# Optimization experiments

Hardware: AMD Instinct MI355X
Metric: run time of the kernel (lower is better)

## Reference

```python
import jax, jax.numpy as jnp
import numpy as np

B, S = 2, 2048
Q_DIM, KV_DIM = 2048, 2048
N_HEADS, HEAD_DIM = 16, 128
N_KV_HEADS = 4            # kv_bandwidth 512 // head_dim 128
N_REP = N_HEADS // N_KV_HEADS
EPS = 1e-5


def setup_inputs() -> dict:
    key = jax.random.key(0)
    ks = jax.random.split(key, 6)
    return {
        "q_stream": jax.random.normal(ks[0], (B, S, Q_DIM), jnp.float32),
        "kv_stream": jax.random.normal(ks[1], (B, S, KV_DIM), jnp.float32),
        "wq": jax.random.normal(ks[2], (Q_DIM, N_HEADS * HEAD_DIM), jnp.float32) * 0.02,
        "wk": jax.random.normal(ks[3], (KV_DIM, N_KV_HEADS * HEAD_DIM), jnp.float32) * 0.02,
        "wv": jax.random.normal(ks[4], (KV_DIM, N_KV_HEADS * HEAD_DIM), jnp.float32) * 0.02,
        "wo": jax.random.normal(ks[5], (N_HEADS * HEAD_DIM, Q_DIM), jnp.float32) * 0.02,
        "q_norm_w": jnp.ones((HEAD_DIM,), jnp.float32),
        "k_norm_w": jnp.ones((HEAD_DIM,), jnp.float32),
    }


def _rmsnorm(x, w):
    # RMSNorm over the last (head_dim) axis
    var = jnp.mean(x * x, axis=-1, keepdims=True)
    return x * jax.lax.rsqrt(var + EPS) * w


def reference(q_stream, kv_stream, wq, wk, wv, wo, q_norm_w, k_norm_w):
    b, s, _ = q_stream.shape
    # QKV projections (weights stored [in, out])
    xq = jnp.einsum("bsd,de->bse", q_stream, wq).reshape(b, s, N_HEADS, HEAD_DIM)
    xk = jnp.einsum("bsd,de->bse", kv_stream, wk).reshape(b, s, N_KV_HEADS, HEAD_DIM)
    xv = jnp.einsum("bsd,de->bse", kv_stream, wv).reshape(b, s, N_KV_HEADS, HEAD_DIM)
    # qk_norm_mode == "before_rope": per-head RMSNorm on q and k
    xq = _rmsnorm(xq, q_norm_w)
    xk = _rmsnorm(xk, k_norm_w)
    # GQA: repeat kv heads to match query heads
    k = jnp.repeat(xk, N_REP, axis=2)  # [b, s, H, D]
    v = jnp.repeat(xv, N_REP, axis=2)
    # causal scaled-dot-product attention
    scale = 1.0 / np.sqrt(HEAD_DIM).astype(np.float32)
    scores = jnp.einsum("bqhd,bkhd->bhqk", xq, k) * scale  # [b, H, S, S]
    causal = jnp.tril(jnp.ones((s, s), dtype=bool))
    scores = jnp.where(causal, scores, jnp.finfo(scores.dtype).min)
    probs = jax.nn.softmax(scores, axis=-1)
    out = jnp.einsum("bhqk,bkhd->bqhd", probs, v).reshape(b, s, N_HEADS * HEAD_DIM)
    return jnp.einsum("bse,eo->bso", out, wo)
```

## Files before the change

### kernel.cpp

```cpp
#include <hip/hip_runtime.h>
#include <cstdint>


using bf16 = __bf16;
using bf16x4 = __attribute__((ext_vector_type(4))) __bf16;
using bf16x8 = __attribute__((ext_vector_type(8))) __bf16;
using s16x4  = __attribute__((ext_vector_type(4))) short;
using f32x4  = __attribute__((ext_vector_type(4))) float;

#define SEQ 2048
#define NH 16
#define NKVH 4
#define HD 128

#define NEG (-3.0e38f)

#if defined(__has_builtin)
#if __has_builtin(__builtin_amdgcn_mfma_f32_16x16x16bf16_1k)
#define HAVE_1K 1
#endif
#endif
__device__ __forceinline__ f32x4 mfma_16x16x16(bf16x4 a, bf16x4 b, f32x4 c) {
#ifdef HAVE_1K
    return __builtin_amdgcn_mfma_f32_16x16x16bf16_1k(
        __builtin_bit_cast(s16x4, a), __builtin_bit_cast(s16x4, b), c, 0, 0, 0);
#else
    f32x4 d;
    asm volatile("v_mfma_f32_16x16x16_bf16 %0, %1, %2, %3"
                 : "=v"(d) : "v"(a), "v"(b), "v"(c));
    return d;
#endif
}

__device__ __forceinline__ float fast_exp2(float x) {
#if defined(__has_builtin)
#if __has_builtin(__builtin_amdgcn_exp2f)
    return __builtin_amdgcn_exp2f(x);
#else
    return exp2f(x);
#endif
#else
    return exp2f(x);
#endif
}

__device__ __forceinline__ void load_lds16(const bf16* g, bf16* l) {
    __builtin_amdgcn_global_load_lds(
        (const __attribute__((address_space(1))) unsigned int*)g,
        (__attribute__((address_space(3))) unsigned int*)l, 16, 0, 0);
}

__global__ __launch_bounds__(256) void cvt_f32_bf16(const float* __restrict__ in,
                                                    bf16* __restrict__ out, int n8) {
    int i = blockIdx.x * 256 + threadIdx.x;
    if (i >= n8) return;
    const float4* p = (const float4*)in + (long)i * 2;
    float4 f0 = p[0], f1 = p[1];
    bf16x8 o = {(bf16)f0.x, (bf16)f0.y, (bf16)f0.z, (bf16)f0.w,
                (bf16)f1.x, (bf16)f1.y, (bf16)f1.z, (bf16)f1.w};
    *((bf16x8*)out + i) = o;
}

__global__ void transpose2d(const float* __restrict__ in, bf16* __restrict__ out,
                            int R, int C) {
    __shared__ bf16 tile[32][33];
    int x  = blockIdx.x * 32 + threadIdx.x;
    int y0 = blockIdx.y * 32 + threadIdx.y;
#pragma unroll
    for (int i = 0; i < 32; i += 8) {
        int y = y0 + i;
        if (y < R && x < C) tile[threadIdx.y + i][threadIdx.x] = (bf16)in[(long)y * C + x];
    }
    __syncthreads();
    int ox  = blockIdx.y * 32 + threadIdx.x;
    int oy0 = blockIdx.x * 32 + threadIdx.y;
#pragma unroll
    for (int i = 0; i < 32; i += 8) {
        int oy = oy0 + i;
        if (oy < C && ox < R) out[(long)oy * R + ox] = tile[threadIdx.x][threadIdx.y + i];
    }
}

template <typename CT>
__global__ __launch_bounds__(256) void gemm_bt(const bf16* __restrict__ A,
                                               const bf16* __restrict__ BT,
                                               CT* __restrict__ C,
                                               int M, int N, int K) {
    __shared__ bf16 As[2][128][32];
    __shared__ bf16 Bs[2][128][32];
    const int tid  = threadIdx.x;
    const int wave = tid >> 6, lane = tid & 63;
    const int nwg = gridDim.x * gridDim.y;
    const int bid = blockIdx.y * gridDim.x + blockIdx.x;
    const int swz = (bid & 7) * (nwg >> 3) + (bid >> 3);
    const int bx = swz % gridDim.x, by = swz / gridDim.x;
    const int m0 = by * 128, n0 = bx * 128;
    const int wm = (wave >> 1) * 64, wn = (wave & 1) * 64;
    const int lrow = lane & 15, quad = lane >> 4;
    const int lko = quad * 8;

    const bf16* ga0 = A  + (long)(m0 + (tid >> 2)) * K + (tid & 3) * 8;
    const bf16* ga1 = ga0 + 64L * K;
    const bf16* gb0 = BT + (long)(n0 + (tid >> 2)) * K + (tid & 3) * 8;
    const bf16* gb1 = gb0 + 64L * K;
    bf16* la0 = &As[0][0][0] + tid * 8;
    bf16* lb0 = &Bs[0][0][0] + tid * 8;

    f32x4 acc[4][4] = {};

    const int nIt = K >> 5;
    load_lds16(ga0, la0);
    load_lds16(ga1, la0 + 2048);
    load_lds16(gb0, lb0);
    load_lds16(gb1, lb0 + 2048);
    __syncthreads();

#pragma unroll 1
    for (int it = 0; it < nIt; ++it) {
        const int cur = it & 1;
        if (it + 1 < nIt) {
            const int k0 = (it + 1) * 32;
            bf16* la = la0 + (cur ^ 1) * 4096;
            bf16* lb = lb0 + (cur ^ 1) * 4096;
            load_lds16(ga0 + k0, la);
            load_lds16(ga1 + k0, la + 2048);
            load_lds16(gb0 + k0, lb);
            load_lds16(gb1 + k0, lb + 2048);
        }
        bf16x8 af[4], bfr[4];
#pragma unroll
        for (int i = 0; i < 4; ++i) af[i]  = *(const bf16x8*)(&As[cur][wm + i * 16 + lrow][lko]);
#pragma unroll
        for (int j = 0; j < 4; ++j) bfr[j] = *(const bf16x8*)(&Bs[cur][wn + j * 16 + lrow][lko]);
#pragma unroll
        for (int i = 0; i < 4; ++i)
#pragma unroll
            for (int j = 0; j < 4; ++j)
                acc[i][j] = __builtin_amdgcn_mfma_f32_16x16x32_bf16(af[i], bfr[j], acc[i][j], 0, 0, 0);
        __syncthreads();
    }
#pragma unroll
    for (int i = 0; i < 4; ++i) {
        int mrow0 = m0 + wm + i * 16 + quad * 4;
#pragma unroll
        for (int j = 0; j < 4; ++j) {
            int ncol = n0 + wn + j * 16 + lrow;
#pragma unroll
            for (int r = 0; r < 4; ++r)
                C[(long)(mrow0 + r) * N + ncol] = (CT)acc[i][j][r];
        }
    }
}

__global__ __launch_bounds__(256) void rmsnorm_head(bf16* __restrict__ X,
                                                    const float* __restrict__ W,
                                                    int nvec, int lhpr, int stride) {
    int v = blockIdx.x * 4 + (threadIdx.x >> 6);
    int lane = threadIdx.x & 63;
    if (v >= nvec) return;
    int row = v >> lhpr, head = v & ((1 << lhpr) - 1);
    bf16* x = X + (long)row * stride + head * HD;
    float fa = (float)x[lane * 2], fb = (float)x[lane * 2 + 1];
    float ss = fa * fa + fb * fb;
#pragma unroll
    for (int off = 1; off < 64; off <<= 1) ss += __shfl_xor(ss, off, 64);
    float r = rsqrtf(ss * (1.0f / 128.0f) + 1e-5f);
    x[lane * 2]     = (bf16)(fa * r * W[lane * 2]);
    x[lane * 2 + 1] = (bf16)(fb * r * W[lane * 2 + 1]);
}

__global__ __launch_bounds__(256) void repack_k(const bf16* __restrict__ xkv,
                                                bf16* __restrict__ kf) {
    int kt = blockIdx.x, kvh = blockIdx.y, b = blockIdx.z;
    int tid = threadIdx.x, lane = tid & 63, ks = tid >> 6;
    int lrow = lane & 15, quad = lane >> 4;
    const bf16* src = xkv + ((long)b * SEQ + kt * 64) * 1024 + kvh * HD;
    bf16* dst = kf + ((long)((b * NKVH + kvh) * 32 + kt)) * 8192;
#pragma unroll
    for (int nt = 0; nt < 4; ++nt) {
        bf16x8 v = *(const bf16x8*)(src + (long)(nt * 16 + lrow) * 1024 + ks * 32 + quad * 8);
        *(bf16x8*)(dst + ((nt * 4 + ks) * 64 + lane) * 8) = v;
    }
}

__global__ __launch_bounds__(256) void repack_v(const bf16* __restrict__ xkv,
                                                bf16* __restrict__ vf) {
    __shared__ bf16 Vls[64][136];
    int kt = blockIdx.x, kvh = blockIdx.y, b = blockIdx.z;
    int tid = threadIdx.x;
    const bf16* src = xkv + ((long)b * SEQ + kt * 64) * 1024 + 512 + kvh * HD;
#pragma unroll
    for (int p = 0; p < 4; ++p) {
        int c = p * 256 + tid;
        int r = c >> 4, dc = (c & 15) * 8;
        *(uint4*)(&Vls[r][dc]) = *(const uint4*)(src + (long)r * 1024 + dc);
    }
    __syncthreads();
    int lane = tid & 63, w = tid >> 6, lrow = lane & 15, quad = lane >> 4;
    bf16* dst = vf + ((long)((b * NKVH + kvh) * 32 + kt)) * 8192;
#pragma unroll
    for (int nt = 0; nt < 4; ++nt)
#pragma unroll
        for (int dtl = 0; dtl < 2; ++dtl) {
            int dt = w * 2 + dtl;
            bf16x4 v = {Vls[nt * 16 + quad * 4 + 0][dt * 16 + lrow],
                        Vls[nt * 16 + quad * 4 + 1][dt * 16 + lrow],
                        Vls[nt * 16 + quad * 4 + 2][dt * 16 + lrow],
                        Vls[nt * 16 + quad * 4 + 3][dt * 16 + lrow]};
            *(bf16x4*)(dst + ((nt * 8 + dt) * 64 + lane) * 4) = v;
        }
}

__global__ __launch_bounds__(512, 4) void attn_kernel(const bf16* __restrict__ Q,
                                                      const bf16* __restrict__ KF,
                                                      const bf16* __restrict__ VF,
                                                      bf16* __restrict__ O) {
    __shared__ bf16 Kf[2][8192];
    __shared__ bf16 Vf[2][8192];
    const int tid = threadIdx.x, wave = tid >> 6, lane = tid & 63;
    const int w4 = wave & 3, grpW = wave >> 2;
    const int bid = blockIdx.x;
    const int grp = bid & 7;
    const int b = grp >> 2, kvh = grp & 3;
    const int slot = bid >> 3;
    const int pr = slot & 15;
    const int h = kvh * 4 + (slot >> 4);
    const int lrow = lane & 15, quad = lane >> 4;
    const float scl2 = 0.12751744f;
    const float THR = 62.7f;

    const int qt1 = 31 - pr, qt2 = pr;

    const bf16* kfb = KF + ((long)(b * NKVH + kvh) * 32) * 8192;
    const bf16* vfb = VF + ((long)(b * NKVH + kvh) * 32) * 8192;

    auto stage = [&](int pair, int bsel) {
        const bf16* kg = kfb + (long)pair * 8192 + tid * 8;
        const bf16* vg = vfb + (long)pair * 8192 + tid * 8;
        bf16* kd = &Kf[bsel][0] + tid * 8;
        bf16* vd = &Vf[bsel][0] + tid * 8;
        load_lds16(kg, kd);
        load_lds16(kg + 4096, kd + 4096);
        load_lds16(vg, vd);
        load_lds16(vg + 4096, vd + 4096);
    };

    float m_i = NEG, l_i = 0.f;
    f32x4 oT[8] = {};
    bf16x8 bqw[4];

    auto combine_write_reset = [&](int qrow) {
        float a1keep = 0.f;
        float* vs = (float*)&Vf[0][0];
        const int sl = w4 * 64 + lane;
        __syncthreads();
        if (grpW == 1) {
            float* d = vs + sl * 18;
#pragma unroll
            for (int dt = 0; dt < 4; ++dt)
#pragma unroll
                for (int r = 0; r < 4; ++r) d[dt * 4 + r] = oT[dt][r];
            d[16] = m_i; d[17] = l_i;
        }
        __syncthreads();
        if (grpW == 0) {
            const float* s = vs + sl * 18;
            float m1 = s[16], l1 = s[17];
            float ms = fmaxf(m_i, m1);
            float a0 = fast_exp2((m_i - ms) * scl2);
            float a1 = fast_exp2((m1 - ms) * scl2);
            a1keep = a1;
            l_i = a0 * l_i + a1 * l1;
#pragma unroll
            for (int dt = 0; dt < 4; ++dt)
#pragma unroll
                for (int r = 0; r < 4; ++r)
                    oT[dt][r] = a0 * oT[dt][r] + a1 * s[dt * 4 + r];
#pragma unroll
            for (int dt = 4; dt < 8; ++dt)
#pragma unroll
                for (int r = 0; r < 4; ++r) oT[dt][r] *= a0;
            m_i = ms;
        }
        __syncthreads();
        if (grpW == 1) {
            float* d = vs + sl * 16;
#pragma unroll
            for (int dt = 4; dt < 8; ++dt)
#pragma unroll
                for (int r = 0; r < 4; ++r) d[(dt - 4) * 4 + r] = oT[dt][r];
        }
        __syncthreads();
        if (grpW == 0) {
            const float* s = vs + sl * 16;
#pragma unroll
            for (int dt = 4; dt < 8; ++dt)
#pragma unroll
                for (int r = 0; r < 4; ++r) oT[dt][r] += a1keep * s[(dt - 4) * 4 + r];
            float inv_l = 1.0f / l_i;
            bf16* obase = O + ((long)(b * SEQ + qrow)) * (NH * HD) + h * HD;
#pragma unroll
            for (int dt = 0; dt < 8; ++dt) {
                bf16x4 o = {(bf16)(oT[dt][0] * inv_l), (bf16)(oT[dt][1] * inv_l),
                            (bf16)(oT[dt][2] * inv_l), (bf16)(oT[dt][3] * inv_l)};
                *(bf16x4*)(obase + dt * 16 + quad * 4) = o;
            }
        }
        __syncthreads();
        m_i = NEG; l_i = 0.f;
#pragma unroll
        for (int dt = 0; dt < 8; ++dt)
#pragma unroll
            for (int r = 0; r < 4; ++r) oT[dt][r] = 0.f;
    };

    auto process = [&](int i, int itN, int myq, int cur) {
        const int kbg = 2 * i + grpW;
        const bool diag = (i == itN - 1);
        const bf16* kbase = &Kf[cur][0] + grpW * 4096;
        const bf16* vbase = &Vf[cur][0] + grpW * 4096;

        f32x4 st[2];
        __builtin_amdgcn_s_setprio(1);
#pragma unroll
        for (int nt = 0; nt < 2; ++nt) {
            f32x4 acc = {};
#pragma unroll
            for (int ks = 0; ks < 4; ++ks) {
                bf16x8 ak = *(const bf16x8*)(kbase + (nt * 4 + ks) * 512 + lane * 8);
                acc = __builtin_amdgcn_mfma_f32_16x16x32_bf16(ak, bqw[ks], acc, 0, 0, 0);
            }
            st[nt] = acc;
        }
        __builtin_amdgcn_s_setprio(0);
        if (diag) {
#pragma unroll
            for (int nt = 0; nt < 2; ++nt) {
                int kp0 = kbg * 32 + nt * 16 + quad * 4;
#pragma unroll
                for (int r = 0; r < 4; ++r)
                    if (kp0 + r > myq) st[nt][r] = NEG;
            }
        }

        float mx = st[0][0];
#pragma unroll
        for (int nt = 0; nt < 2; ++nt)
#pragma unroll
            for (int r = 0; r < 4; ++r) mx = fmaxf(mx, st[nt][r]);
        mx = fmaxf(mx, __shfl_xor(mx, 16, 64));
        mx = fmaxf(mx, __shfl_xor(mx, 32, 64));

        if (!__all(mx - m_i <= THR)) {
            float mnew = fmaxf(m_i, mx);
            float alpha = fast_exp2((m_i - mnew) * scl2);
            l_i *= alpha;
#pragma unroll
            for (int dt = 0; dt < 8; ++dt)
#pragma unroll
                for (int r = 0; r < 4; ++r) oT[dt][r] *= alpha;
            m_i = mnew;
        }
        float rs = 0.f;
#pragma unroll
        for (int nt = 0; nt < 2; ++nt)
#pragma unroll
            for (int r = 0; r < 4; ++r) {
                float p = fast_exp2((st[nt][r] - m_i) * scl2);
                st[nt][r] = p;
                rs += p;
            }
        rs += __shfl_xor(rs, 16, 64);
        rs += __shfl_xor(rs, 32, 64);
        l_i += rs;

        bf16x4 pf[2];
#pragma unroll
        for (int nt = 0; nt < 2; ++nt) {
            bf16x4 tt = {(bf16)st[nt][0], (bf16)st[nt][1],
                         (bf16)st[nt][2], (bf16)st[nt][3]};
            pf[nt] = tt;
        }

        __builtin_amdgcn_s_setprio(1);
#pragma unroll
        for (int nt = 0; nt < 2; ++nt)
#pragma unroll
            for (int dt = 0; dt < 8; ++dt) {
                bf16x4 av = *(const bf16x4*)(vbase + (nt * 8 + dt) * 256 + lane * 4);
                oT[dt] = mfma_16x16x16(av, pf[nt], oT[dt]);
            }
        __builtin_amdgcn_s_setprio(0);
    };

    const int it1 = qt1 + 1;
    const int myq1 = qt1 * 64 + w4 * 16 + lrow;
    {
        const bf16* qrow = Q + ((long)(b * SEQ + myq1)) * (NH * HD) + h * HD;
#pragma unroll
        for (int ks = 0; ks < 4; ++ks)
            bqw[ks] = *(const bf16x8*)(qrow + ks * 32 + quad * 8);
    }
    stage(0, 0);
    __syncthreads();
#pragma unroll 1
    for (int i = 0; i < it1; ++i) {
        const int cur = i & 1;
        if (i + 1 < it1) stage(i + 1, cur ^ 1);
        process(i, it1, myq1, cur);
        __syncthreads();
    }
    combine_write_reset(myq1);

    const int it2 = qt2 + 1;
    const int myq2 = qt2 * 64 + w4 * 16 + lrow;
    {
        const bf16* qrow = Q + ((long)(b * SEQ + myq2)) * (NH * HD) + h * HD;
#pragma unroll
        for (int ks = 0; ks < 4; ++ks)
            bqw[ks] = *(const bf16x8*)(qrow + ks * 32 + quad * 8);
    }
    stage(0, 0);
    __syncthreads();
#pragma unroll 1
    for (int i = 0; i < it2; ++i) {
        const int cur = i & 1;
        if (i + 1 < it2) stage(i + 1, cur ^ 1);
        process(i, it2, myq2, cur);
        __syncthreads();
    }
    combine_write_reset(qt2 * 64 + w4 * 16 + lrow);
}

extern "C" void kernel_launch(void* const* d_in, const int* in_sizes, int n_in,
                              void* d_out, int out_size, void* d_ws, size_t ws_size,
                              hipStream_t stream) {
    const float* q_stream  = (const float*)d_in[0];
    const float* kv_stream = (const float*)d_in[1];
    const float* wq  = (const float*)d_in[2];
    const float* wk  = (const float*)d_in[3];
    const float* wv  = (const float*)d_in[4];
    const float* wo  = (const float*)d_in[5];
    const float* qnw = (const float*)d_in[6];
    const float* knw = (const float*)d_in[7];
    float* out = (float*)d_out;

    bf16* ws   = (bf16*)d_ws;
    bf16* sb   = ws;
    bf16* wqT  = ws + 8L * 1024 * 1024;
    bf16* wkvT = wqT + 4L * 1024 * 1024;
    bf16* xq   = wkvT + 2L * 1024 * 1024;
    bf16* xkv  = xq + 8L * 1024 * 1024;
    bf16* kf   = xkv + 4L * 1024 * 1024;
    bf16* vf   = kf + 2L * 1024 * 1024;

    dim3 tb(32, 8);
    cvt_f32_bf16<<<4096, 256, 0, stream>>>(q_stream, sb, 1048576);
    transpose2d<<<dim3(64, 64), tb, 0, stream>>>(wq, wqT, 2048, 2048);
    transpose2d<<<dim3(16, 64), tb, 0, stream>>>(wk, wkvT, 2048, 512);
    transpose2d<<<dim3(16, 64), tb, 0, stream>>>(wv, wkvT + 512L * 2048, 2048, 512);
    gemm_bt<bf16><<<dim3(16, 32), 256, 0, stream>>>(sb, wqT, xq, 4096, 2048, 2048);
    cvt_f32_bf16<<<4096, 256, 0, stream>>>(kv_stream, sb, 1048576);
    transpose2d<<<dim3(64, 64), tb, 0, stream>>>(wo, wqT, 2048, 2048);
    gemm_bt<bf16><<<dim3(8, 32), 256, 0, stream>>>(sb, wkvT, xkv, 4096, 1024, 2048);
    rmsnorm_head<<<(4096 * 16) / 4, 256, 0, stream>>>(xq, qnw, 4096 * 16, 4, 2048);
    rmsnorm_head<<<(4096 * 4) / 4, 256, 0, stream>>>(xkv, knw, 4096 * 4, 2, 1024);
    repack_k<<<dim3(32, 4, 2), 256, 0, stream>>>(xkv, kf);
    repack_v<<<dim3(32, 4, 2), 256, 0, stream>>>(xkv, vf);
    attn_kernel<<<dim3(512), dim3(512), 0, stream>>>(xq, kf, vf, sb);
    gemm_bt<float><<<dim3(16, 32), 256, 0, stream>>>(sb, wqT, out, 4096, 2048, 2048);

    (void)in_sizes; (void)n_in; (void)out_size; (void)ws_size;
}
```

Before: 384.9 us.

## Triple-buffer GEMM LDS staging with partial vmcnt waits

Replaces the double-buffered LDS pipeline in the bf16 GEMM with a three-stage ring buffer that prefetches two K-tiles ahead. It waits only for the oldest tile's loads (vmcnt(4)) before the barrier instead of draining all outstanding loads. The goal is to keep more global-to-LDS traffic in flight and hide memory latency behind the MFMA work. In exchange LDS use per block grows from 32KB to 48KB, which may reduce occupancy, and correctness now depends on load_lds16 emitting exactly one vmem op per call.

```diff
diff --git a/kernel.cpp b/kernel.cpp
--- a/kernel.cpp
+++ b/kernel.cpp
@@ -86,8 +86,8 @@
                                                const bf16* __restrict__ BT,
                                                CT* __restrict__ C,
                                                int M, int N, int K) {
-    __shared__ bf16 As[2][128][32];
-    __shared__ bf16 Bs[2][128][32];
+    __shared__ bf16 As[3][128][32];
+    __shared__ bf16 Bs[3][128][32];
     const int tid  = threadIdx.x;
     const int wave = tid >> 6, lane = tid & 63;
     const int nwg = gridDim.x * gridDim.y;
@@ -106,27 +106,35 @@
     bf16* la0 = &As[0][0][0] + tid * 8;
     bf16* lb0 = &Bs[0][0][0] + tid * 8;
 
+    auto stg = [&](int it) {
+        const int j = it % 3;
+        const int k0 = it * 32;
+        bf16* la = la0 + j * 4096;
+        bf16* lb = lb0 + j * 4096;
+        load_lds16(ga0 + k0, la);
+        load_lds16(ga1 + k0, la + 2048);
+        load_lds16(gb0 + k0, lb);
+        load_lds16(gb1 + k0, lb + 2048);
+    };
+
     f32x4 acc[4][4] = {};
-
     const int nIt = K >> 5;
-    load_lds16(ga0, la0);
-    load_lds16(ga1, la0 + 2048);
-    load_lds16(gb0, lb0);
-    load_lds16(gb1, lb0 + 2048);
-    __syncthreads();
-
+
+    stg(0);
+    if (nIt > 1) {
+        stg(1);
+        asm volatile("s_waitcnt vmcnt(4)" ::: "memory");
+    } else {
+        asm volatile("s_waitcnt vmcnt(0)" ::: "memory");
+    }
+    __builtin_amdgcn_s_barrier();
+    __builtin_amdgcn_sched_barrier(0);
+
+    int cur = 0;
 #pragma unroll 1
     for (int it = 0; it < nIt; ++it) {
-        const int cur = it & 1;
-        if (it + 1 < nIt) {
-            const int k0 = (it + 1) * 32;
-            bf16* la = la0 + (cur ^ 1) * 4096;
-            bf16* lb = lb0 + (cur ^ 1) * 4096;
-            load_lds16(ga0 + k0, la);
-            load_lds16(ga1 + k0, la + 2048);
-            load_lds16(gb0 + k0, lb);
-            load_lds16(gb1 + k0, lb + 2048);
-        }
+        const bool pre = (it + 2 < nIt);
+        if (pre) stg(it + 2);
         bf16x8 af[4], bfr[4];
 #pragma unroll
         for (int i = 0; i < 4; ++i) af[i]  = *(const bf16x8*)(&As[cur][wm + i * 16 + lrow][lko]);
@@ -137,7 +145,11 @@
 #pragma unroll
             for (int j = 0; j < 4; ++j)
                 acc[i][j] = __builtin_amdgcn_mfma_f32_16x16x32_bf16(af[i], bfr[j], acc[i][j], 0, 0, 0);
-        __syncthreads();
+        if (pre) asm volatile("s_waitcnt vmcnt(4)" ::: "memory");
+        else     asm volatile("s_waitcnt vmcnt(0)" ::: "memory");
+        __builtin_amdgcn_s_barrier();
+        __builtin_amdgcn_sched_barrier(0);
+        cur = (cur == 2) ? 0 : cur + 1;
     }
 #pragma unroll
     for (int i = 0; i < 4; ++i) {
@@ -429,7 +441,7 @@
         process(i, it2, myq2, cur);
         __syncthreads();
     }
-    combine_write_reset(qt2 * 64 + w4 * 16 + lrow);
+    combine_write_reset(myq2);
 }
 
 extern "C" void kernel_launch(void* const* d_in, const int* in_sizes, int n_in,
```

Result: no change. 389.4 us (+1.2%).
